# Optimization experiments

Measured on AMD Instinct MI355X. Metric: run time of the kernel, lower is better.

Reference implementation:

```python
import jax, jax.numpy as jnp
import numpy as np

EMB_DIM = 512
HEAD_DIM = 512


def setup_inputs() -> dict:
    key = jax.random.key(0)
    ks = jax.random.split(key, 7)
    B, S = 4, 2048
    lim = 1.0 / np.sqrt(EMB_DIM)  # torch Linear default init range
    x = jax.random.normal(ks[0], (B, S, EMB_DIM), dtype=jnp.float32)
    Wq = jax.random.uniform(ks[1], (HEAD_DIM, EMB_DIM), jnp.float32, -lim, lim)
    Wk = jax.random.uniform(ks[2], (HEAD_DIM, EMB_DIM), jnp.float32, -lim, lim)
    Wv = jax.random.uniform(ks[3], (HEAD_DIM, EMB_DIM), jnp.float32, -lim, lim)
    bq = jax.random.uniform(ks[4], (HEAD_DIM,), jnp.float32, -lim, lim)
    bk = jax.random.uniform(ks[5], (HEAD_DIM,), jnp.float32, -lim, lim)
    bv = jax.random.uniform(ks[6], (HEAD_DIM,), jnp.float32, -lim, lim)
    return {"x": x, "Wq": Wq, "bq": bq, "Wk": Wk, "bk": bk, "Wv": Wv, "bv": bv}


def reference(x, Wq, bq, Wk, bk, Wv, bv):
    # torch nn.Linear: y = x @ W.T + b
    q = jnp.einsum('bse,de->bsd', x, Wq) + bq
    k = jnp.einsum('bse,de->bsd', x, Wk) + bk
    v = jnp.einsum('bse,de->bsd', x, Wv) + bv
    scale = jnp.sqrt(jnp.asarray(HEAD_DIM, dtype=q.dtype))
    scores = jnp.einsum('bqd,bkd->bqk', q, k) / scale  # [B,S,S]
    S = x.shape[1]
    causal = jnp.triu(jnp.ones((S, S), dtype=bool), k=1)  # True above diagonal
    scores = jnp.where(causal[None, :, :], -jnp.inf, scores)
    attn = jax.nn.softmax(scores, axis=-1)
    return jnp.einsum('bqk,bkd->bqd', attn, v)
```

## Files before the change

### kernel.cpp

```cpp
#include <hip/hip_runtime.h>
#include <hip/hip_bf16.h>
#include <cstdint>
#include <math.h>

#define S_LEN 2048
#define D_DIM 512
#define NROWS 8192
#define NQKV  1536
#define QK_SCALE 0.04419417382415922f

typedef unsigned short u16;
typedef unsigned long long u64;
typedef __attribute__((ext_vector_type(8))) short short8;
typedef __attribute__((ext_vector_type(4))) float floatx4;

__device__ inline floatx4 mfma16(short8 a, short8 b, floatx4 c){
  return __builtin_amdgcn_mfma_f32_16x16x32_bf16(a, b, c, 0, 0, 0);
}
__device__ inline u16 f2b(float f){
  uint32_t u = __float_as_uint(f);
  u = (u + 0x7fffu + ((u >> 16) & 1u)) >> 16;
  return (u16)u;
}
__device__ inline float b2f(u16 u){ return __uint_as_float(((uint32_t)u) << 16); }
#define GLD16(g, l) __builtin_amdgcn_global_load_lds( \
    (const __attribute__((address_space(1))) void*)(g), \
    (__attribute__((address_space(3))) void*)(l), 16, 0, 0)

__global__ void cvt_kernel(const float* __restrict__ x,
                           const float* __restrict__ Wq,
                           const float* __restrict__ Wk,
                           const float* __restrict__ Wv,
                           u16* __restrict__ xw)
{
  const int NT4 = (NROWS * D_DIM) / 4 + (NQKV * D_DIM) / 4;
  for (int i = blockIdx.x * blockDim.x + threadIdx.x; i < NT4;
       i += gridDim.x * blockDim.x) {
    int e = i * 4;
    const float* src;
    if (e < NROWS * D_DIM) {
      src = x + e;
    } else {
      int j = e - NROWS * D_DIM;
      if (j < 512 * 512)           src = Wq + j;
      else if (j < 2 * 512 * 512)  src = Wk + (j - 512 * 512);
      else                         src = Wv + (j - 2 * 512 * 512);
    }
    float4 v = *(const float4*)src;
    ushort4 o;
    o.x = f2b(v.x); o.y = f2b(v.y); o.z = f2b(v.z); o.w = f2b(v.w);
    *(ushort4*)(xw + e) = o;
  }
}

__launch_bounds__(256)
__global__ void qkv_gemm(const u16* __restrict__ xb,
                         const u16* __restrict__ wb,
                         const float* __restrict__ bq,
                         const float* __restrict__ bk,
                         const float* __restrict__ bv,
                         u16* __restrict__ qb,
                         u16* __restrict__ kb,
                         u16* __restrict__ vt)
{
  __shared__ alignas(16) u16 sm[2][16384];
  const int tid = threadIdx.x;
  const int l = tid & 63, w = tid >> 6;
  const int lr = l & 15, lg = l >> 4;
  const int wr = w >> 1, wc = w & 1;
  const int kx = (lr & 7) << 4;
  const int csw = ((tid & 7) * 16) ^ (((tid >> 3) & 7) << 4);
  const int bid = blockIdx.x;
  const int xcd = bid & 7;
  const int t = bid >> 3;
  const int bn = t % 12, bmhi = t / 12;
  const int bm = (bmhi << 3) | xcd;
  const int m0 = bm * 128, n0 = bn * 128;

  const u16* gA = xb + (size_t)(m0 + (tid >> 3)) * D_DIM + (csw >> 1);
  const u16* gB = wb + (size_t)(n0 + (tid >> 3)) * D_DIM + (csw >> 1);

#define STAGEK(BUF, KT) { \
  char* la = (char*)&sm[BUF][0] + tid * 16; \
  char* lb = (char*)&sm[BUF][8192] + tid * 16; \
  const u16* ga = gA + (KT) * 64; \
  const u16* gb = gB + (KT) * 64; \
  _Pragma("unroll") for (int jj = 0; jj < 4; jj++) { \
    GLD16(ga + (size_t)jj * 32 * D_DIM, la + jj * 4096); \
    GLD16(gb + (size_t)jj * 32 * D_DIM, lb + jj * 4096); } }

  floatx4 acc[4][4];
#pragma unroll
  for (int m = 0; m < 4; m++)
#pragma unroll
    for (int n = 0; n < 4; n++) acc[m][n] = 0.0f;

  STAGEK(0, 0)
  __syncthreads();

  for (int kt = 0; kt < 8; ++kt) {
    const int cb = kt & 1;
    if (kt < 7) STAGEK(cb ^ 1, kt + 1)
#pragma unroll
    for (int kk = 0; kk < 2; ++kk) {
      short8 a[4], bfr[4];
#pragma unroll
      for (int m = 0; m < 4; m++)
        a[m] = *(const short8*)((const char*)&sm[cb][0]
                + (wr * 64 + m * 16 + lr) * 128 + ((kk * 64 + lg * 16) ^ kx));
#pragma unroll
      for (int n = 0; n < 4; n++)
        bfr[n] = *(const short8*)((const char*)&sm[cb][0] + 16384
                + (wc * 64 + n * 16 + lr) * 128 + ((kk * 64 + lg * 16) ^ kx));
#pragma unroll
      for (int m = 0; m < 4; m++)
#pragma unroll
        for (int n = 0; n < 4; n++)
          acc[m][n] = mfma16(a[m], bfr[n], acc[m][n]);
    }
    __syncthreads();
  }
#undef STAGEK

  if (n0 < 1024) {
    const float* bias = (n0 < 512) ? bq : bk;
    u16* dst = (n0 < 512) ? qb : kb;
    const float scl = (n0 < 512) ? QK_SCALE : 1.0f;
    const int nbase = n0 & 511;
#pragma unroll
    for (int n = 0; n < 4; n++) {
      int gn = nbase + wc * 64 + n * 16 + lr;
      float bia = bias[gn];
#pragma unroll
      for (int m = 0; m < 4; m++) {
        int gm0 = m0 + wr * 64 + m * 16 + lg * 4;
#pragma unroll
        for (int r = 0; r < 4; r++)
          dst[(size_t)(gm0 + r) * D_DIM + gn] = f2b((acc[m][n][r] + bia) * scl);
      }
    }
  } else {
    const int nbase = n0 - 1024;
    const int bIdx = m0 >> 11;
    const int s0 = m0 & 2047;
    __syncthreads();
#pragma unroll
    for (int h = 0; h < 2; ++h) {
      if (wc == h) {
#pragma unroll
        for (int n = 0; n < 4; n++) {
          int lrow = n * 16 + lr;
          float bia = bv[nbase + h * 64 + lrow];
#pragma unroll
          for (int m = 0; m < 4; m++) {
            int lcol = wr * 64 + m * 16 + lg * 4;
#pragma unroll
            for (int r = 0; r < 4; r++)
              sm[0][lrow * 136 + lcol + r] = f2b(acc[m][n][r] + bia);
          }
        }
      }
      __syncthreads();
      {
        int row = tid >> 2;
        int c0 = (tid & 3) * 32;
        u16* dstp = vt + (size_t)bIdx * D_DIM * S_LEN
                       + (size_t)(nbase + h * 64 + row) * S_LEN + s0 + c0;
        const u16* srcp = &sm[0][row * 136 + c0];
#pragma unroll
        for (int jj = 0; jj < 4; jj++)
          *(short8*)(dstp + jj * 8) = *(const short8*)(srcp + jj * 8);
      }
      __syncthreads();
    }
  }
}

__launch_bounds__(256)
__global__ void s_gemm(const u16* __restrict__ qb,
                       const u16* __restrict__ kb,
                       u16* __restrict__ P,
                       float* __restrict__ pRS)
{
  __shared__ alignas(16) u16 sm[2][16384];
  const int tid = threadIdx.x;
  const int l = tid & 63, w = tid >> 6;
  const int lr = l & 15, lg = l >> 4;
  const int wr = w >> 1, wc = w & 1;
  const int kx = (lr & 7) << 4;
  const int csw = ((tid & 7) * 16) ^ (((tid >> 3) & 7) << 4);
  const int bid = blockIdx.x;
  const int xcd = bid & 7;
  const int b = xcd >> 1;
  const int j = (bid >> 3) * 2 + (xcd & 1);
  float g = sqrtf(8.f * (float)j + 1.f);
  int qt = (int)((g - 1.f) * 0.5f + 1e-4f);
  while ((qt + 1) * (qt + 2) / 2 <= j) ++qt;
  while (qt * (qt + 1) / 2 > j) --qt;
  const int kt = j - qt * (qt + 1) / 2;

  const u16* gA = kb + ((size_t)(b * S_LEN + kt * 128 + (tid >> 3))) * D_DIM + (csw >> 1);
  const u16* gB = qb + ((size_t)(b * S_LEN + qt * 128 + (tid >> 3))) * D_DIM + (csw >> 1);

#define STAGES(BUF, KT) { \
  char* la = (char*)&sm[BUF][0] + tid * 16; \
  char* lb = (char*)&sm[BUF][8192] + tid * 16; \
  const u16* ga = gA + (KT) * 64; \
  const u16* gb = gB + (KT) * 64; \
  _Pragma("unroll") for (int jj = 0; jj < 4; jj++) { \
    GLD16(ga + (size_t)jj * 32 * D_DIM, la + jj * 4096); \
    GLD16(gb + (size_t)jj * 32 * D_DIM, lb + jj * 4096); } }

  floatx4 acc[4][4];
#pragma unroll
  for (int m = 0; m < 4; m++)
#pragma unroll
    for (int n = 0; n < 4; n++) acc[m][n] = 0.0f;

  STAGES(0, 0)
  __syncthreads();
  for (int ks = 0; ks < 8; ++ks) {
    const int cb = ks & 1;
    if (ks < 7) STAGES(cb ^ 1, ks + 1)
#pragma unroll
    for (int kk = 0; kk < 2; ++kk) {
      short8 a[4], bfr[4];
#pragma unroll
      for (int m = 0; m < 4; m++)
        a[m] = *(const short8*)((const char*)&sm[cb][0]
                + (wr * 64 + m * 16 + lr) * 128 + ((kk * 64 + lg * 16) ^ kx));
#pragma unroll
      for (int n = 0; n < 4; n++)
        bfr[n] = *(const short8*)((const char*)&sm[cb][0] + 16384
                + (wc * 64 + n * 16 + lr) * 128 + ((kk * 64 + lg * 16) ^ kx));
#pragma unroll
      for (int m = 0; m < 4; m++)
#pragma unroll
        for (int n = 0; n < 4; n++)
          acc[m][n] = mfma16(a[m], bfr[n], acc[m][n]);
    }
    __syncthreads();
  }
#undef STAGES

  const bool diag = (kt == qt);
  u16* Pb = P + (size_t)b * S_LEN * S_LEN;
#pragma unroll
  for (int n = 0; n < 4; ++n) {
    const int q = qt * 128 + wc * 64 + n * 16 + lr;
    float rs = 0.f;
#pragma unroll
    for (int m = 0; m < 4; ++m) {
      const int kb0 = kt * 128 + wr * 64 + m * 16 + lg * 4;
      u16 h[4];
#pragma unroll
      for (int r = 0; r < 4; ++r) {
        float e = __expf(acc[m][n][r]);
        if (diag && (kb0 + r > q)) e = 0.f;
        h[r] = f2b(e);
        rs += b2f(h[r]);
      }
      u64 pk = (u64)h[0] | ((u64)h[1] << 16) | ((u64)h[2] << 32) | ((u64)h[3] << 48);
      *(u64*)(Pb + (size_t)q * S_LEN + kb0) = pk;
    }
    rs += __shfl_xor(rs, 16);
    rs += __shfl_xor(rs, 32);
    if (lg == 0)
      pRS[(size_t)(b * S_LEN + q) * 32 + kt * 2 + wr] = rs;
  }
}

__launch_bounds__(256)
__global__ void pv_gemm(const u16* __restrict__ P,
                       const float* __restrict__ pRS,
                       const u16* __restrict__ vt,
                       float* __restrict__ out)
{
  __shared__ alignas(16) u16 sm[2][12288];
  __shared__ float rinv[64];

  const int tid = threadIdx.x;
  const int l = tid & 63, w = tid >> 6;
  const int lr = l & 15, lg = l >> 4;
  const int wr = w >> 1, wc = w & 1;
  const int kx = (lr & 7) << 4;
  const int csw = ((tid & 7) * 16) ^ (((tid >> 3) & 7) << 4);
  const int bid = blockIdx.x;
  const int xcd = bid & 7;
  const int b = xcd >> 1, xl = xcd & 1;
  const int t = bid >> 3;
  const int m = t & 3;
  const int qraw = ((t >> 2) << 1) | xl;
  const int qt = 31 - qraw;
  const int m0 = m * 128;
  const int q0 = qt * 64;
  const int nks = qt + 1;

  const u16* gA = vt + (size_t)b * D_DIM * S_LEN
                     + (size_t)(m0 + (tid >> 3)) * S_LEN + (csw >> 1);
  const u16* gB = P + (size_t)b * S_LEN * S_LEN
                    + (size_t)(q0 + (tid >> 3)) * S_LEN + (csw >> 1);

  {
    const int qi = tid >> 2;
    const int qrow = q0 + qi;
    const int ns = ((qrow >> 7) + 1) * 2;
    float s = 0.f;
    for (int ss = tid & 3; ss < ns; ss += 4)
      s += pRS[(size_t)(b * S_LEN + qrow) * 32 + ss];
    s += __shfl_xor(s, 1);
    s += __shfl_xor(s, 2);
    if ((tid & 3) == 0) rinv[qi] = 1.0f / s;
  }

#define STAGEPV(BUF, KS) { \
  char* la = (char*)&sm[BUF][0] + tid * 16; \
  char* lb = (char*)&sm[BUF][8192] + tid * 16; \
  const u16* ga = gA + (KS) * 64; \
  const u16* gb = gB + (KS) * 64; \
  _Pragma("unroll") for (int jj = 0; jj < 4; jj++) \
    GLD16(ga + (size_t)jj * 32 * S_LEN, la + jj * 4096); \
  _Pragma("unroll") for (int jj = 0; jj < 2; jj++) \
    GLD16(gb + (size_t)jj * 32 * S_LEN, lb + jj * 4096); }

  floatx4 acc[4][2];
#pragma unroll
  for (int mm = 0; mm < 4; mm++) { acc[mm][0] = 0.0f; acc[mm][1] = 0.0f; }

  STAGEPV(0, 0)
  __syncthreads();
  for (int ks = 0; ks < nks; ++ks) {
    const int cb = ks & 1;
    if (ks < nks - 1) STAGEPV(cb ^ 1, ks + 1)
#pragma unroll
    for (int kk = 0; kk < 2; ++kk) {
      short8 a[4], bfr[2];
#pragma unroll
      for (int mm = 0; mm < 4; mm++)
        a[mm] = *(const short8*)((const char*)&sm[cb][0]
                + (wr * 64 + mm * 16 + lr) * 128 + ((kk * 64 + lg * 16) ^ kx));
#pragma unroll
      for (int n = 0; n < 2; n++)
        bfr[n] = *(const short8*)((const char*)&sm[cb][0] + 16384
                + (wc * 32 + n * 16 + lr) * 128 + ((kk * 64 + lg * 16) ^ kx));
#pragma unroll
      for (int mm = 0; mm < 4; mm++)
#pragma unroll
        for (int n = 0; n < 2; n++)
          acc[mm][n] = mfma16(a[mm], bfr[n], acc[mm][n]);
    }
    __syncthreads();
  }
#undef STAGEPV

#pragma unroll
  for (int n = 0; n < 2; ++n) {
    const int q = q0 + wc * 32 + n * 16 + lr;
    const float inv = rinv[wc * 32 + n * 16 + lr];
    float* op = out + (size_t)(b * S_LEN + q) * D_DIM + m0 + wr * 64 + lg * 4;
#pragma unroll
    for (int mm = 0; mm < 4; ++mm) {
      float4 v;
      v.x = acc[mm][n][0] * inv;
      v.y = acc[mm][n][1] * inv;
      v.z = acc[mm][n][2] * inv;
      v.w = acc[mm][n][3] * inv;
      *(float4*)(op + mm * 16) = v;
    }
  }
}

extern "C" void kernel_launch(void* const* d_in, const int* in_sizes, int n_in,
                              void* d_out, int out_size, void* d_ws, size_t ws_size,
                              hipStream_t stream)
{
  const float* x  = (const float*)d_in[0];
  const float* Wq = (const float*)d_in[1];
  const float* bq = (const float*)d_in[2];
  const float* Wk = (const float*)d_in[3];
  const float* bk = (const float*)d_in[4];
  const float* Wv = (const float*)d_in[5];
  const float* bv = (const float*)d_in[6];
  float* out = (float*)d_out;

  u16* xw = (u16*)d_ws;
  u16* xb = xw;
  u16* wb = xb + (size_t)NROWS * D_DIM;
  u16* qb = wb + (size_t)NQKV * D_DIM;
  u16* kb = qb + (size_t)NROWS * D_DIM;
  u16* vt = kb + (size_t)NROWS * D_DIM;
  u16* P  = vt + (size_t)NROWS * D_DIM;
  float* pRS = (float*)(P + (size_t)4 * S_LEN * S_LEN);

  hipLaunchKernelGGL(cvt_kernel, dim3(2048), dim3(256), 0, stream, x, Wq, Wk, Wv, xw);
  hipLaunchKernelGGL(qkv_gemm, dim3(768), dim3(256), 0, stream,
                     xb, wb, bq, bk, bv, qb, kb, vt);
  hipLaunchKernelGGL(s_gemm, dim3(544), dim3(256), 0, stream, qb, kb, P, pRS);
  hipLaunchKernelGGL(pv_gemm, dim3(512), dim3(256), 0, stream, P, pRS, vt, out);
}
```

Measured before the change: 78.92 us.

## Replace double-buffered LDS staging with single buffer in QKV and score GEMMs

Both GEMM kernels drop the two-stage LDS ping-pong and load each K-slice into a single 32KB buffer, syncing before compute and after it. This halves shared memory per block, which could let more blocks sit on each CU. In exchange, global-to-LDS loads no longer overlap the MFMA work of the previous slice, so each block spends more time waiting on loads.

```diff
diff --git a/kernel.cpp b/kernel.cpp
--- a/kernel.cpp
+++ b/kernel.cpp
@@ -63,7 +63,7 @@
                          u16* __restrict__ kb,
                          u16* __restrict__ vt)
 {
-  __shared__ alignas(16) u16 sm[2][16384];
+  __shared__ alignas(16) u16 sm[16384];
   const int tid = threadIdx.x;
   const int l = tid & 63, w = tid >> 6;
   const int lr = l & 15, lg = l >> 4;
@@ -80,9 +80,9 @@
   const u16* gA = xb + (size_t)(m0 + (tid >> 3)) * D_DIM + (csw >> 1);
   const u16* gB = wb + (size_t)(n0 + (tid >> 3)) * D_DIM + (csw >> 1);
 
-#define STAGEK(BUF, KT) { \
-  char* la = (char*)&sm[BUF][0] + tid * 16; \
-  char* lb = (char*)&sm[BUF][8192] + tid * 16; \
+#define STAGEK(KT) { \
+  char* la = (char*)&sm[0] + tid * 16; \
+  char* lb = (char*)&sm[8192] + tid * 16; \
   const u16* ga = gA + (KT) * 64; \
   const u16* gb = gB + (KT) * 64; \
   _Pragma("unroll") for (int jj = 0; jj < 4; jj++) { \
@@ -95,22 +95,19 @@
 #pragma unroll
     for (int n = 0; n < 4; n++) acc[m][n] = 0.0f;
 
-  STAGEK(0, 0)
-  __syncthreads();
-
   for (int kt = 0; kt < 8; ++kt) {
-    const int cb = kt & 1;
-    if (kt < 7) STAGEK(cb ^ 1, kt + 1)
+    STAGEK(kt)
+    __syncthreads();
 #pragma unroll
     for (int kk = 0; kk < 2; ++kk) {
       short8 a[4], bfr[4];
 #pragma unroll
       for (int m = 0; m < 4; m++)
-        a[m] = *(const short8*)((const char*)&sm[cb][0]
+        a[m] = *(const short8*)((const char*)&sm[0]
                 + (wr * 64 + m * 16 + lr) * 128 + ((kk * 64 + lg * 16) ^ kx));
 #pragma unroll
       for (int n = 0; n < 4; n++)
-        bfr[n] = *(const short8*)((const char*)&sm[cb][0] + 16384
+        bfr[n] = *(const short8*)((const char*)&sm[0] + 16384
                 + (wc * 64 + n * 16 + lr) * 128 + ((kk * 64 + lg * 16) ^ kx));
 #pragma unroll
       for (int m = 0; m < 4; m++)
@@ -143,7 +140,6 @@
     const int nbase = n0 - 1024;
     const int bIdx = m0 >> 11;
     const int s0 = m0 & 2047;
-    __syncthreads();
 #pragma unroll
     for (int h = 0; h < 2; ++h) {
       if (wc == h) {
@@ -156,7 +152,7 @@
             int lcol = wr * 64 + m * 16 + lg * 4;
 #pragma unroll
             for (int r = 0; r < 4; r++)
-              sm[0][lrow * 136 + lcol + r] = f2b(acc[m][n][r] + bia);
+              sm[lrow * 136 + lcol + r] = f2b(acc[m][n][r] + bia);
           }
         }
       }
@@ -166,7 +162,7 @@
         int c0 = (tid & 3) * 32;
         u16* dstp = vt + (size_t)bIdx * D_DIM * S_LEN
                        + (size_t)(nbase + h * 64 + row) * S_LEN + s0 + c0;
-        const u16* srcp = &sm[0][row * 136 + c0];
+        const u16* srcp = &sm[row * 136 + c0];
 #pragma unroll
         for (int jj = 0; jj < 4; jj++)
           *(short8*)(dstp + jj * 8) = *(const short8*)(srcp + jj * 8);
@@ -182,7 +178,7 @@
                        u16* __restrict__ P,
                        float* __restrict__ pRS)
 {
-  __shared__ alignas(16) u16 sm[2][16384];
+  __shared__ alignas(16) u16 sm[16384];
   const int tid = threadIdx.x;
   const int l = tid & 63, w = tid >> 6;
   const int lr = l & 15, lg = l >> 4;
@@ -202,9 +198,9 @@
   const u16* gA = kb + ((size_t)(b * S_LEN + kt * 128 + (tid >> 3))) * D_DIM + (csw >> 1);
   const u16* gB = qb + ((size_t)(b * S_LEN + qt * 128 + (tid >> 3))) * D_DIM + (csw >> 1);
 
-#define STAGES(BUF, KT) { \
-  char* la = (char*)&sm[BUF][0] + tid * 16; \
-  char* lb = (char*)&sm[BUF][8192] + tid * 16; \
+#define STAGES(KT) { \
+  char* la = (char*)&sm[0] + tid * 16; \
+  char* lb = (char*)&sm[8192] + tid * 16; \
   const u16* ga = gA + (KT) * 64; \
   const u16* gb = gB + (KT) * 64; \
   _Pragma("unroll") for (int jj = 0; jj < 4; jj++) { \
@@ -217,21 +213,19 @@
 #pragma unroll
     for (int n = 0; n < 4; n++) acc[m][n] = 0.0f;
 
-  STAGES(0, 0)
-  __syncthreads();
   for (int ks = 0; ks < 8; ++ks) {
-    const int cb = ks & 1;
-    if (ks < 7) STAGES(cb ^ 1, ks + 1)
+    STAGES(ks)
+    __syncthreads();
 #pragma unroll
     for (int kk = 0; kk < 2; ++kk) {
       short8 a[4], bfr[4];
 #pragma unroll
       for (int m = 0; m < 4; m++)
-        a[m] = *(const short8*)((const char*)&sm[cb][0]
+        a[m] = *(const short8*)((const char*)&sm[0]
                 + (wr * 64 + m * 16 + lr) * 128 + ((kk * 64 + lg * 16) ^ kx));
 #pragma unroll
       for (int n = 0; n < 4; n++)
-        bfr[n] = *(const short8*)((const char*)&sm[cb][0] + 16384
+        bfr[n] = *(const short8*)((const char*)&sm[0] + 16384
                 + (wc * 64 + n * 16 + lr) * 128 + ((kk * 64 + lg * 16) ^ kx));
 #pragma unroll
       for (int m = 0; m < 4; m++)
```

Result: slower. 93.54 us (+18.5%).

## Fuse fp32-to-bf16 conversion of x into QKV GEMM A-tile staging

Applied to the files above, without the earlier changes.

The separate conversion pass over the activation x is dropped. The QKV GEMM now loads fp32 x tiles into registers, converts them to bf16, and writes them into LDS after the MFMA work, so the next tile's loads overlap compute. This removes one full write and read of an 8 MB bf16 copy of x, plus part of the conversion kernel. In exchange, the GEMM reads twice the A bytes, since each x tile is re-read in fp32 by every N-tile block. It also adds register pressure and VALU conversion work inside the main loop.

```diff
diff --git a/kernel.cpp b/kernel.cpp
--- a/kernel.cpp
+++ b/kernel.cpp
@@ -27,34 +27,28 @@
     (const __attribute__((address_space(1))) void*)(g), \
     (__attribute__((address_space(3))) void*)(l), 16, 0, 0)
 
-__global__ void cvt_kernel(const float* __restrict__ x,
-                           const float* __restrict__ Wq,
+__global__ void cvt_kernel(const float* __restrict__ Wq,
                            const float* __restrict__ Wk,
                            const float* __restrict__ Wv,
-                           u16* __restrict__ xw)
+                           u16* __restrict__ wb)
 {
-  const int NT4 = (NROWS * D_DIM) / 4 + (NQKV * D_DIM) / 4;
+  const int NT4 = (NQKV * D_DIM) / 4;
   for (int i = blockIdx.x * blockDim.x + threadIdx.x; i < NT4;
        i += gridDim.x * blockDim.x) {
     int e = i * 4;
     const float* src;
-    if (e < NROWS * D_DIM) {
-      src = x + e;
-    } else {
-      int j = e - NROWS * D_DIM;
-      if (j < 512 * 512)           src = Wq + j;
-      else if (j < 2 * 512 * 512)  src = Wk + (j - 512 * 512);
-      else                         src = Wv + (j - 2 * 512 * 512);
-    }
+    if (e < 512 * 512)           src = Wq + e;
+    else if (e < 2 * 512 * 512)  src = Wk + (e - 512 * 512);
+    else                         src = Wv + (e - 2 * 512 * 512);
     float4 v = *(const float4*)src;
     ushort4 o;
     o.x = f2b(v.x); o.y = f2b(v.y); o.z = f2b(v.z); o.w = f2b(v.w);
-    *(ushort4*)(xw + e) = o;
+    *(ushort4*)(wb + e) = o;
   }
 }
 
 __launch_bounds__(256)
-__global__ void qkv_gemm(const u16* __restrict__ xb,
+__global__ void qkv_gemm(const float* __restrict__ x,
                          const u16* __restrict__ wb,
                          const float* __restrict__ bq,
                          const float* __restrict__ bk,
@@ -77,17 +71,32 @@
   const int bm = (bmhi << 3) | xcd;
   const int m0 = bm * 128, n0 = bn * 128;
 
-  const u16* gA = xb + (size_t)(m0 + (tid >> 3)) * D_DIM + (csw >> 1);
+  const float* gAf = x + (size_t)(m0 + (tid >> 3)) * D_DIM + (csw >> 1);
   const u16* gB = wb + (size_t)(n0 + (tid >> 3)) * D_DIM + (csw >> 1);
 
-#define STAGEK(BUF, KT) { \
+  float4 va0[4], va1[4];
+
+#define LOADA(KT) { \
+  const float* pa = gAf + (KT) * 64; \
+  _Pragma("unroll") for (int jj = 0; jj < 4; jj++) { \
+    va0[jj] = *(const float4*)(pa + (size_t)jj * 32 * D_DIM); \
+    va1[jj] = *(const float4*)(pa + (size_t)jj * 32 * D_DIM + 4); } }
+
+#define WRITEA(BUF) { \
   char* la = (char*)&sm[BUF][0] + tid * 16; \
+  _Pragma("unroll") for (int jj = 0; jj < 4; jj++) { \
+    short8 h; \
+    h[0] = (short)f2b(va0[jj].x); h[1] = (short)f2b(va0[jj].y); \
+    h[2] = (short)f2b(va0[jj].z); h[3] = (short)f2b(va0[jj].w); \
+    h[4] = (short)f2b(va1[jj].x); h[5] = (short)f2b(va1[jj].y); \
+    h[6] = (short)f2b(va1[jj].z); h[7] = (short)f2b(va1[jj].w); \
+    *(short8*)(la + jj * 4096) = h; } }
+
+#define STAGEB(BUF, KT) { \
   char* lb = (char*)&sm[BUF][8192] + tid * 16; \
-  const u16* ga = gA + (KT) * 64; \
   const u16* gb = gB + (KT) * 64; \
-  _Pragma("unroll") for (int jj = 0; jj < 4; jj++) { \
-    GLD16(ga + (size_t)jj * 32 * D_DIM, la + jj * 4096); \
-    GLD16(gb + (size_t)jj * 32 * D_DIM, lb + jj * 4096); } }
+  _Pragma("unroll") for (int jj = 0; jj < 4; jj++) \
+    GLD16(gb + (size_t)jj * 32 * D_DIM, lb + jj * 4096); }
 
   floatx4 acc[4][4];
 #pragma unroll
@@ -95,12 +104,17 @@
 #pragma unroll
     for (int n = 0; n < 4; n++) acc[m][n] = 0.0f;
 
-  STAGEK(0, 0)
+  LOADA(0)
+  WRITEA(0)
+  STAGEB(0, 0)
   __syncthreads();
 
   for (int kt = 0; kt < 8; ++kt) {
     const int cb = kt & 1;
-    if (kt < 7) STAGEK(cb ^ 1, kt + 1)
+    if (kt < 7) {
+      LOADA(kt + 1)
+      STAGEB(cb ^ 1, kt + 1)
+    }
 #pragma unroll
     for (int kk = 0; kk < 2; ++kk) {
       short8 a[4], bfr[4];
@@ -118,9 +132,12 @@
         for (int n = 0; n < 4; n++)
           acc[m][n] = mfma16(a[m], bfr[n], acc[m][n]);
     }
+    if (kt < 7) WRITEA(cb ^ 1)
     __syncthreads();
   }
-#undef STAGEK
+#undef LOADA
+#undef WRITEA
+#undef STAGEB
 
   if (n0 < 1024) {
     const float* bias = (n0 < 512) ? bq : bk;
@@ -384,17 +401,16 @@
   float* out = (float*)d_out;
 
   u16* xw = (u16*)d_ws;
-  u16* xb = xw;
-  u16* wb = xb + (size_t)NROWS * D_DIM;
+  u16* wb = xw;
   u16* qb = wb + (size_t)NQKV * D_DIM;
   u16* kb = qb + (size_t)NROWS * D_DIM;
   u16* vt = kb + (size_t)NROWS * D_DIM;
   u16* P  = vt + (size_t)NROWS * D_DIM;
   float* pRS = (float*)(P + (size_t)4 * S_LEN * S_LEN);
 
-  hipLaunchKernelGGL(cvt_kernel, dim3(2048), dim3(256), 0, stream, x, Wq, Wk, Wv, xw);
+  hipLaunchKernelGGL(cvt_kernel, dim3(512), dim3(256), 0, stream, Wq, Wk, Wv, wb);
   hipLaunchKernelGGL(qkv_gemm, dim3(768), dim3(256), 0, stream,
-                     xb, wb, bq, bk, bv, qb, kb, vt);
+                     x, wb, bq, bk, bv, qb, kb, vt);
   hipLaunchKernelGGL(s_gemm, dim3(544), dim3(256), 0, stream, qb, kb, P, pRS);
   hipLaunchKernelGGL(pv_gemm, dim3(512), dim3(256), 0, stream, P, pRS, vt, out);
 }
```

After: 89.61 us. 1.14x slower.

## Split-K the long causal PV tiles and add a reduction kernel

Applied to the files above, without the earlier changes.

The PV GEMM now splits the K range of the heavier half of query tiles (qt>=16) into two blocks, raising the grid from 512 to 768 blocks to even out the causal load imbalance. Partial results are written as bf16 to a workspace and a new pv_reduce kernel sums the two halves, normalizes by the row sums and writes fp32 output. This costs an extra launch, extra global traffic, and some precision loss from rounding the partials to bf16.

```diff
diff --git a/kernel.cpp b/kernel.cpp
--- a/kernel.cpp
+++ b/kernel.cpp
@@ -274,7 +274,8 @@
 __global__ void pv_gemm(const u16* __restrict__ P,
                        const float* __restrict__ pRS,
                        const u16* __restrict__ vt,
-                       float* __restrict__ out)
+                       float* __restrict__ out,
+                       u16* __restrict__ pOp)
 {
   __shared__ alignas(16) u16 sm[2][12288];
   __shared__ float rinv[64];
@@ -288,20 +289,36 @@
   const int bid = blockIdx.x;
   const int xcd = bid & 7;
   const int b = xcd >> 1, xl = xcd & 1;
-  const int t = bid >> 3;
-  const int m = t & 3;
-  const int qraw = ((t >> 2) << 1) | xl;
-  const int qt = 31 - qraw;
+  const int j = (bid >> 3) * 2 + xl;
+
+  int qt, m, c0k, nsteps, slot;
+  if (j < 128) {
+    const int cc = j & 1;
+    const int mq = j >> 1;
+    m = mq & 3;
+    qt = 31 - (mq >> 2);
+    const int nks = qt + 1;
+    const int half = (nks + 1) >> 1;
+    c0k = cc ? half : 0;
+    nsteps = cc ? (nks - half) : half;
+    slot = (((b * 16 + (qt - 16)) * 4 + m) << 1) | cc;
+  } else {
+    const int jj = j - 128;
+    m = jj & 3;
+    qt = 15 - (jj >> 2);
+    c0k = 0;
+    nsteps = qt + 1;
+    slot = -1;
+  }
   const int m0 = m * 128;
   const int q0 = qt * 64;
-  const int nks = qt + 1;
 
   const u16* gA = vt + (size_t)b * D_DIM * S_LEN
-                     + (size_t)(m0 + (tid >> 3)) * S_LEN + (csw >> 1);
+                     + (size_t)(m0 + (tid >> 3)) * S_LEN + c0k * 64 + (csw >> 1);
   const u16* gB = P + (size_t)b * S_LEN * S_LEN
-                    + (size_t)(q0 + (tid >> 3)) * S_LEN + (csw >> 1);
-
-  {
+                    + (size_t)(q0 + (tid >> 3)) * S_LEN + c0k * 64 + (csw >> 1);
+
+  if (slot < 0) {
     const int qi = tid >> 2;
     const int qrow = q0 + qi;
     const int ns = ((qrow >> 7) + 1) * 2;
@@ -329,9 +346,9 @@
 
   STAGEPV(0, 0)
   __syncthreads();
-  for (int ks = 0; ks < nks; ++ks) {
+  for (int ks = 0; ks < nsteps; ++ks) {
     const int cb = ks & 1;
-    if (ks < nks - 1) STAGEPV(cb ^ 1, ks + 1)
+    if (ks < nsteps - 1) STAGEPV(cb ^ 1, ks + 1)
 #pragma unroll
     for (int kk = 0; kk < 2; ++kk) {
       short8 a[4], bfr[2];
@@ -353,20 +370,75 @@
   }
 #undef STAGEPV
 
-#pragma unroll
-  for (int n = 0; n < 2; ++n) {
-    const int q = q0 + wc * 32 + n * 16 + lr;
-    const float inv = rinv[wc * 32 + n * 16 + lr];
-    float* op = out + (size_t)(b * S_LEN + q) * D_DIM + m0 + wr * 64 + lg * 4;
-#pragma unroll
-    for (int mm = 0; mm < 4; ++mm) {
-      float4 v;
-      v.x = acc[mm][n][0] * inv;
-      v.y = acc[mm][n][1] * inv;
-      v.z = acc[mm][n][2] * inv;
-      v.w = acc[mm][n][3] * inv;
-      *(float4*)(op + mm * 16) = v;
-    }
+  if (slot >= 0) {
+    u16* po = pOp + (size_t)slot * 8192;
+#pragma unroll
+    for (int n = 0; n < 2; ++n) {
+      const int row = wc * 32 + n * 16 + lr;
+#pragma unroll
+      for (int mm = 0; mm < 4; ++mm) {
+        const int dloc = wr * 64 + mm * 16 + lg * 4;
+        u64 pk = (u64)f2b(acc[mm][n][0]) | ((u64)f2b(acc[mm][n][1]) << 16)
+               | ((u64)f2b(acc[mm][n][2]) << 32) | ((u64)f2b(acc[mm][n][3]) << 48);
+        __builtin_nontemporal_store(pk, (u64*)(po + row * 128 + dloc));
+      }
+    }
+  } else {
+#pragma unroll
+    for (int n = 0; n < 2; ++n) {
+      const int q = q0 + wc * 32 + n * 16 + lr;
+      const float inv = rinv[wc * 32 + n * 16 + lr];
+      float* op = out + (size_t)(b * S_LEN + q) * D_DIM + m0 + wr * 64 + lg * 4;
+#pragma unroll
+      for (int mm = 0; mm < 4; ++mm) {
+        float4 v;
+        v.x = acc[mm][n][0] * inv;
+        v.y = acc[mm][n][1] * inv;
+        v.z = acc[mm][n][2] * inv;
+        v.w = acc[mm][n][3] * inv;
+        *(float4*)(op + mm * 16) = v;
+      }
+    }
+  }
+}
+
+__launch_bounds__(256)
+__global__ void pv_reduce(const u16* __restrict__ pOp,
+                          const float* __restrict__ pRS,
+                          float* __restrict__ out)
+{
+  const int id = blockIdx.x;
+  const int m = id & 3;
+  const int qq = (id >> 2) & 15;
+  const int b = id >> 6;
+  const int qt = 16 + qq;
+  const int q0 = qt * 64;
+  const int m0 = m * 128;
+  const int sbase = id * 2;
+
+  const int row = threadIdx.x >> 2;
+  const int col0 = (threadIdx.x & 3) * 32;
+  const int qrow = q0 + row;
+
+  const int ns = ((qrow >> 7) + 1) * 2;
+  float s = 0.f;
+  for (int ss = 0; ss < ns; ++ss)
+    s += pRS[(size_t)(b * S_LEN + qrow) * 32 + ss];
+  const float inv = 1.0f / s;
+
+  const u16* s0p = pOp + (size_t)sbase * 8192 + row * 128 + col0;
+  const u16* s1p = s0p + 8192;
+  float* dst = out + (size_t)(b * S_LEN + qrow) * D_DIM + m0 + col0;
+#pragma unroll
+  for (int jj = 0; jj < 8; ++jj) {
+    ushort4 a = ((const ushort4*)s0p)[jj];
+    ushort4 c = ((const ushort4*)s1p)[jj];
+    float4 v;
+    v.x = (b2f(a.x) + b2f(c.x)) * inv;
+    v.y = (b2f(a.y) + b2f(c.y)) * inv;
+    v.z = (b2f(a.z) + b2f(c.z)) * inv;
+    v.w = (b2f(a.w) + b2f(c.w)) * inv;
+    *(float4*)(dst + jj * 4) = v;
   }
 }
 
@@ -391,10 +463,12 @@
   u16* vt = kb + (size_t)NROWS * D_DIM;
   u16* P  = vt + (size_t)NROWS * D_DIM;
   float* pRS = (float*)(P + (size_t)4 * S_LEN * S_LEN);
+  u16* pOp = (u16*)(pRS + (size_t)NROWS * 32);
 
   hipLaunchKernelGGL(cvt_kernel, dim3(2048), dim3(256), 0, stream, x, Wq, Wk, Wv, xw);
   hipLaunchKernelGGL(qkv_gemm, dim3(768), dim3(256), 0, stream,
                      xb, wb, bq, bk, bv, qb, kb, vt);
   hipLaunchKernelGGL(s_gemm, dim3(544), dim3(256), 0, stream, qb, kb, P, pRS);
-  hipLaunchKernelGGL(pv_gemm, dim3(512), dim3(256), 0, stream, P, pRS, vt, out);
-}
+  hipLaunchKernelGGL(pv_gemm, dim3(768), dim3(256), 0, stream, P, pRS, vt, out, pOp);
+  hipLaunchKernelGGL(pv_reduce, dim3(256), dim3(256), 0, stream, pOp, pRS, out);
+}
```

After: 78.59 us, median of 2. Within noise of the previous version (-0.4%).
